# Kernel optimization log

Measured on AMD Instinct MI355X. Metric: run time of the kernel, lower is better.

The kernel has to match this reference:

```python
import jax, jax.numpy as jnp
import numpy as np

B, T, C = 2, 2048, 1024
H, D = 16, 64


def setup_inputs() -> dict:
    key = jax.random.key(0)
    ks = jax.random.split(key, 6)
    s = 0.02
    return {
        "x": jax.random.normal(ks[0], (B, T, C), dtype=jnp.float32),
        "W_qkv": jax.random.normal(ks[1], (3 * H * D, C), dtype=jnp.float32) * s,
        "b_qkv": jnp.zeros((3 * H * D,), dtype=jnp.float32),
        "W_proj": jax.random.normal(ks[2], (C, H * D), dtype=jnp.float32) * s,
        "b_proj": jnp.zeros((C,), dtype=jnp.float32),
        "sink_logit": jnp.zeros((H,), dtype=jnp.float32),
    }


def reference(x, W_qkv, b_qkv, W_proj, b_proj, sink_logit):
    Bx, Tx, Cx = x.shape
    qkv = x @ W_qkv.T + b_qkv  # (B,T,3*H*D)
    q, k, v = jnp.split(qkv, 3, axis=-1)
    # (B,T,H,D) -> (B,H,T,D)
    q = q.reshape(Bx, Tx, H, D).transpose(0, 2, 1, 3)
    k = k.reshape(Bx, Tx, H, D).transpose(0, 2, 1, 3)
    v = v.reshape(Bx, Tx, H, D).transpose(0, 2, 1, 3)
    scale = 1.0 / jnp.sqrt(jnp.asarray(D, dtype=x.dtype))
    scores = jnp.einsum("bhqd,bhkd->bhqk", q, k) * scale  # (B,H,T,T)
    neg_inf = jnp.finfo(x.dtype).min
    causal = jnp.tril(jnp.ones((Tx, Tx), dtype=bool))
    scores = jnp.where(causal[None, None], scores, neg_inf)
    # sink slot: k_sink = 0 so its logit is just the learnable sink bias
    sink = jnp.broadcast_to(sink_logit[None, :, None, None], (Bx, H, Tx, 1))
    logits = jnp.concatenate([sink.astype(scores.dtype), scores], axis=-1)  # (B,H,T,T+1)
    probs = jax.nn.softmax(logits, axis=-1)
    # v_sink is zero, so drop sink column in the value contraction
    out = jnp.einsum("bhqk,bhkd->bhqd", probs[..., 1:], v)
    y = out.transpose(0, 2, 1, 3).reshape(Bx, Tx, H * D)
    return y @ W_proj.T + b_proj
```

## Files before the change

### kernel.cpp

```cpp
#include <hip/hip_runtime.h>
#include <hip/hip_bf16.h>

#define Bb 2
#define Tt 2048
#define Cc 1024
#define Hh 16
#define Dd 64

typedef __bf16 bf8 __attribute__((ext_vector_type(8)));
typedef __bf16 bf4 __attribute__((ext_vector_type(4)));
typedef float f4 __attribute__((ext_vector_type(4)));

typedef __attribute__((address_space(3))) void lds_void;
typedef const __attribute__((address_space(1))) void g_void;

__device__ __forceinline__ void gload_lds16(const __bf16* g, __bf16* l) {
  __builtin_amdgcn_global_load_lds((g_void*)g, (lds_void*)l, 16, 0, 0);
}

__device__ __forceinline__ float ex2(float x) { return __builtin_amdgcn_exp2f(x); }

__global__ __launch_bounds__(256) void cvt3_kernel(
    const float* __restrict__ a, __bf16* __restrict__ oa, int na,
    const float* __restrict__ b, __bf16* __restrict__ ob, int nb,
    const float* __restrict__ c, __bf16* __restrict__ oc) {
  int gi = blockIdx.x * 256 + threadIdx.x;
  const int t0 = na >> 3, t1 = t0 + (nb >> 3);
  const float* src; __bf16* dst; int idx;
  if (gi < t0)      { src = a; dst = oa; idx = gi; }
  else if (gi < t1) { src = b; dst = ob; idx = gi - t0; }
  else              { src = c; dst = oc; idx = gi - t1; }
  const float* p = src + (size_t)idx * 8;
  float4 u = *(const float4*)p;
  float4 v = *(const float4*)(p + 4);
  bf8 r;
  r[0] = (__bf16)u.x; r[1] = (__bf16)u.y; r[2] = (__bf16)u.z; r[3] = (__bf16)u.w;
  r[4] = (__bf16)v.x; r[5] = (__bf16)v.y; r[6] = (__bf16)v.z; r[7] = (__bf16)v.w;
  *(bf8*)(dst + (size_t)idx * 8) = r;
}

__global__ __launch_bounds__(256) void gemm128_kernel(
    const __bf16* __restrict__ A, const __bf16* __restrict__ W,
    const float* __restrict__ bias, int K, int mode,
    __bf16* __restrict__ q_ws, __bf16* __restrict__ k_ws,
    __bf16* __restrict__ v_ws, float* __restrict__ out, int ldo)
{
  const int tid = threadIdx.x;
  const int lane = tid & 63, wave = tid >> 6;
  const int lr = lane & 15, lq = lane >> 4;
  const int m_blk = blockIdx.y * 128, n_blk = blockIdx.x * 128;
  const int wm = (wave & 1) * 64, wn = (wave >> 1) * 64;

  __shared__ __align__(16) __bf16 As[128 * 32];
  __shared__ __align__(16) __bf16 Bs[128 * 32];

  const int srow = tid >> 2, scol = (tid & 3) * 8;
  const __bf16* ag0 = A + (size_t)(m_blk + srow) * K + scol;
  const __bf16* ag1 = A + (size_t)(m_blk + 64 + srow) * K + scol;
  const __bf16* bg0 = W + (size_t)(n_blk + srow) * K + scol;
  const __bf16* bg1 = W + (size_t)(n_blk + 64 + srow) * K + scol;
  __bf16* al0 = As + tid * 8;
  __bf16* al1 = As + 2048 + tid * 8;
  __bf16* bl0 = Bs + tid * 8;
  __bf16* bl1 = Bs + 2048 + tid * 8;

  f4 acc[4][4] = {};
  for (int k0 = 0; k0 < K; k0 += 32) {
    gload_lds16(ag0 + k0, al0);
    gload_lds16(ag1 + k0, al1);
    gload_lds16(bg0 + k0, bl0);
    gload_lds16(bg1 + k0, bl1);
    __syncthreads();

    bf8 af[4], bfr[4];
    #pragma unroll
    for (int i = 0; i < 4; ++i)
      af[i] = *(const bf8*)&As[(wm + i * 16 + lr) * 32 + lq * 8];
    #pragma unroll
    for (int j = 0; j < 4; ++j)
      bfr[j] = *(const bf8*)&Bs[(wn + j * 16 + lr) * 32 + lq * 8];
    #pragma unroll
    for (int i = 0; i < 4; ++i)
      #pragma unroll
      for (int j = 0; j < 4; ++j)
        acc[i][j] = __builtin_amdgcn_mfma_f32_16x16x32_bf16(af[i], bfr[j], acc[i][j], 0, 0, 0);
    __syncthreads();
  }

  #pragma unroll
  for (int i = 0; i < 4; ++i) {
    #pragma unroll
    for (int j = 0; j < 4; ++j) {
      #pragma unroll
      for (int r = 0; r < 4; ++r) {
        int row = m_blk + wm + i * 16 + lq * 4 + r;
        int col = n_blk + wn + j * 16 + lr;
        float val = acc[i][j][r] + bias[col];
        if (mode == 0) {
          int which = col >> 10, rr = col & 1023;
          int h = rr >> 6, d = rr & 63;
          int b = row >> 11, t = row & 2047;
          if (which == 0) val *= 0.18033688011112042f;
          __bf16 bv = (__bf16)val;
          size_t bh = (size_t)b * Hh + h;
          if (which == 0)      q_ws[(bh * Tt + t) * Dd + d] = bv;
          else if (which == 1) k_ws[(bh * Tt + t) * Dd + d] = bv;
          else                 v_ws[(bh * Dd + d) * Tt + t] = bv;
        } else {
          out[(size_t)row * ldo + col] = val;
        }
      }
    }
  }
}

__global__ __launch_bounds__(256) void attn_kernel(
    const __bf16* __restrict__ q_ws, const __bf16* __restrict__ k_ws,
    const __bf16* __restrict__ v_ws, const float* __restrict__ sink,
    __bf16* __restrict__ y_ws)
{
  int bi = blockIdx.x;
  int qt, bhi;
  if (bi < 256) { qt = 15 - (bi >> 5); bhi = bi & 31; }
  else          { qt = (bi - 256) >> 5; bhi = (bi - 256) & 31; }
  const int h = bhi & (Hh - 1);
  const int b = bhi >> 4;
  const int tid = threadIdx.x;
  const int lane = tid & 63, wave = tid >> 6;
  const int lr = lane & 15, lq = lane >> 4;

  __shared__ __align__(16) __bf16 KsU[3][64 * 64];
  __shared__ __align__(16) __bf16 VtU[3][64 * 64];
  __shared__ __align__(16) __bf16 PsU[4][2 * 16 * 64];

  const __bf16* qp = q_ws + (size_t)bhi * Tt * Dd;
  const __bf16* kp = k_ws + (size_t)bhi * Tt * Dd;
  const __bf16* vp = v_ws + (size_t)bhi * Dd * Tt;

  const int qbase = qt * 128;
  const int qlo = qbase + wave * 32;

  bf8 qf[2][2];
  #pragma unroll
  for (int qs = 0; qs < 2; ++qs) {
    const __bf16* qrow = qp + (size_t)(qlo + qs * 16 + lr) * Dd;
    qf[qs][0] = *(const bf8*)(qrow + lq * 8);
    qf[qs][1] = *(const bf8*)(qrow + 32 + lq * 8);
  }

  float rs[2] = {0.f, 0.f};
  f4 o_acc[2][4] = {};

  const int srow_lo = wave * 8 + (lane >> 3);
  const int sslot = lane & 7;
  const int nkt = 2 * qt + 2;

  auto stage = [&](int kt2, int bsel) {
    const int kbase2 = kt2 * 64;
    #pragma unroll
    for (int ii = 0; ii < 2; ++ii) {
      const int r = ii * 32 + srow_lo;
      const int cc = sslot ^ (r & 7);
      gload_lds16(kp + (size_t)(kbase2 + r) * Dd + cc * 8,
                  &KsU[bsel][ii * 2048 + wave * 512 + lane * 8]);
      gload_lds16(vp + (size_t)r * Tt + kbase2 + cc * 8,
                  &VtU[bsel][ii * 2048 + wave * 512 + lane * 8]);
    }
  };

  auto computeS = [&](const __bf16* Kb, f4 (&sA)[4][2]) {
    #pragma unroll
    for (int nt = 0; nt < 4; ++nt) {
      const int krow = nt * 16 + lr;
      const int x7 = krow & 7;
      bf8 kb0 = *(const bf8*)&Kb[krow * 64 + ((lq ^ x7) * 8)];
      bf8 kb1 = *(const bf8*)&Kb[krow * 64 + (((4 + lq) ^ x7) * 8)];
      #pragma unroll
      for (int qs = 0; qs < 2; ++qs) {
        f4 c = {};
        c = __builtin_amdgcn_mfma_f32_16x16x32_bf16(kb0, qf[qs][0], c, 0, 0, 0);
        c = __builtin_amdgcn_mfma_f32_16x16x32_bf16(kb1, qf[qs][1], c, 0, 0, 0);
        sA[nt][qs] = c;
      }
    }
  };

  f4 s_cur[4][2], s_next[4][2];

  stage(0, 0);
  __syncthreads();
  stage(1, 1);
  computeS(KsU[0], s_cur);

  for (int kt = 0; kt < nkt; ++kt) {
    __syncthreads();
    if (kt + 2 < nkt) stage(kt + 2, (kt + 2) % 3);

    if (kt + 1 < nkt && (kt + 1) * 64 <= qlo + 31)
      computeS(KsU[(kt + 1) % 3], s_next);

    const int kbase = kt * 64;
    if (kbase <= qlo + 31) {
      __bf16* Pw = PsU[wave];
      const bool diag = (kbase + 63 > qlo);
      if (diag) {
        #pragma unroll
        for (int nt = 0; nt < 4; ++nt)
          #pragma unroll
          for (int qs = 0; qs < 2; ++qs) {
            const int qg = qlo + qs * 16 + lr;
            const int kg = kbase + nt * 16 + lq * 4;
            bf4 pb;
            #pragma unroll
            for (int r = 0; r < 4; ++r) {
              float sv = (kg + r > qg) ? -1e30f : s_cur[nt][qs][r];
              float p = ex2(sv);
              rs[qs] += p;
              pb[r] = (__bf16)p;
            }
            const int G = (nt * 2 + (lq >> 1)) ^ (lr & 7);
            *(bf4*)&Pw[(qs * 16 + lr) * 64 + G * 8 + (lq & 1) * 4] = pb;
          }
      } else {
        #pragma unroll
        for (int nt = 0; nt < 4; ++nt)
          #pragma unroll
          for (int qs = 0; qs < 2; ++qs) {
            bf4 pb;
            #pragma unroll
            for (int r = 0; r < 4; ++r) {
              float p = ex2(s_cur[nt][qs][r]);
              rs[qs] += p;
              pb[r] = (__bf16)p;
            }
            const int G = (nt * 2 + (lq >> 1)) ^ (lr & 7);
            *(bf4*)&Pw[(qs * 16 + lr) * 64 + G * 8 + (lq & 1) * 4] = pb;
          }
      }
      asm volatile("s_waitcnt lgkmcnt(0)" ::: "memory");

      const __bf16* Vb = VtU[kt % 3];
      #pragma unroll
      for (int ks = 0; ks < 2; ++ks) {
        const int pg = ((ks * 4 + lq) ^ (lr & 7)) * 8;
        bf8 pa0 = *(const bf8*)&Pw[lr * 64 + pg];
        bf8 pa1 = *(const bf8*)&Pw[(16 + lr) * 64 + pg];
        #pragma unroll
        for (int dt = 0; dt < 4; ++dt) {
          const int vrow = dt * 16 + lr;
          bf8 vb = *(const bf8*)&Vb[vrow * 64 + (((ks * 4 + lq) ^ (vrow & 7)) * 8)];
          o_acc[0][dt] = __builtin_amdgcn_mfma_f32_16x16x32_bf16(pa0, vb, o_acc[0][dt], 0, 0, 0);
          o_acc[1][dt] = __builtin_amdgcn_mfma_f32_16x16x32_bf16(pa1, vb, o_acc[1][dt], 0, 0, 0);
        }
      }
    }

    #pragma unroll
    for (int nt = 0; nt < 4; ++nt)
      #pragma unroll
      for (int qs = 0; qs < 2; ++qs)
        s_cur[nt][qs] = s_next[nt][qs];
  }

  #pragma unroll
  for (int qs = 0; qs < 2; ++qs) {
    rs[qs] += __shfl_xor(rs[qs], 16, 64);
    rs[qs] += __shfl_xor(rs[qs], 32, 64);
  }
  const float snk = ex2(sink[h] * 1.44269504f);
  float inv0 = 1.0f / (rs[0] + snk);
  float inv1 = 1.0f / (rs[1] + snk);
  float invr[2][4];
  #pragma unroll
  for (int r = 0; r < 4; ++r) {
    invr[0][r] = __shfl(inv0, lq * 4 + r, 64);
    invr[1][r] = __shfl(inv1, lq * 4 + r, 64);
  }

  #pragma unroll
  for (int qs = 0; qs < 2; ++qs)
    #pragma unroll
    for (int dt = 0; dt < 4; ++dt)
      #pragma unroll
      for (int r = 0; r < 4; ++r) {
        int qrow = qbase + wave * 32 + qs * 16 + lq * 4 + r;
        y_ws[((size_t)b * Tt + qrow) * Cc + h * Dd + dt * 16 + lr] =
            (__bf16)(o_acc[qs][dt][r] * invr[qs][r]);
      }
}

extern "C" void kernel_launch(void* const* d_in, const int* in_sizes, int n_in,
                              void* d_out, int out_size, void* d_ws, size_t ws_size,
                              hipStream_t stream) {
  const float* x      = (const float*)d_in[0];
  const float* W_qkv  = (const float*)d_in[1];
  const float* b_qkv  = (const float*)d_in[2];
  const float* W_proj = (const float*)d_in[3];
  const float* b_proj = (const float*)d_in[4];
  const float* sinkp  = (const float*)d_in[5];
  float* out = (float*)d_out;

  const size_t n_x    = (size_t)Bb * Tt * Cc;
  const size_t n_wqkv = (size_t)3 * Hh * Dd * Cc;
  const size_t n_wprj = (size_t)Cc * Hh * Dd;
  const size_t nqkv   = (size_t)Bb * Hh * Tt * Dd;

  __bf16* xb     = (__bf16*)d_ws;
  __bf16* wqkvb  = xb + n_x;
  __bf16* wprojb = wqkvb + n_wqkv;
  __bf16* q_ws   = wprojb + n_wprj;
  __bf16* k_ws   = q_ws + nqkv;
  __bf16* v_ws   = k_ws + nqkv;
  __bf16* y_ws   = xb;

  dim3 blk(256);
  const int cvt_blocks = (int)((n_x + n_wqkv + n_wprj) / 8 / 256);
  cvt3_kernel<<<cvt_blocks, blk, 0, stream>>>(x, xb, (int)n_x,
                                              W_qkv, wqkvb, (int)n_wqkv,
                                              W_proj, wprojb);

  gemm128_kernel<<<dim3(3 * Cc / 128, Bb * Tt / 128), blk, 0, stream>>>(
      xb, wqkvb, b_qkv, Cc, 0, q_ws, k_ws, v_ws, nullptr, 0);
  attn_kernel<<<dim3(512), blk, 0, stream>>>(q_ws, k_ws, v_ws, sinkp, y_ws);
  gemm128_kernel<<<dim3(Cc / 128, Bb * Tt / 128), blk, 0, stream>>>(
      y_ws, wprojb, b_proj, Hh * Dd, 1, nullptr, nullptr, nullptr, out, Cc);
}
```

Before: 203.7 us.

## Double-buffer GEMM LDS tiles, swizzle LDS layout, use 64-row tiles for projection

```diff
diff --git a/kernel.cpp b/kernel.cpp
--- a/kernel.cpp
+++ b/kernel.cpp
@@ -39,64 +39,87 @@
   *(bf8*)(dst + (size_t)idx * 8) = r;
 }
 
-__global__ __launch_bounds__(256) void gemm128_kernel(
+template<int BM, int BN, int MODE>
+__global__ __launch_bounds__(256) void gemm_kernel(
     const __bf16* __restrict__ A, const __bf16* __restrict__ W,
-    const float* __restrict__ bias, int K, int mode,
+    const float* __restrict__ bias, int K,
     __bf16* __restrict__ q_ws, __bf16* __restrict__ k_ws,
     __bf16* __restrict__ v_ws, float* __restrict__ out, int ldo)
 {
+  constexpr int WM = (BM == 128) ? 64 : 32;
+  constexpr int WN = 64;
+  constexpr int WAVES_M = BM / WM;
+  constexpr int MI = WM / 16, NI = WN / 16;
+  constexpr int NA = BM / 64, NB = BN / 64;
+
   const int tid = threadIdx.x;
   const int lane = tid & 63, wave = tid >> 6;
   const int lr = lane & 15, lq = lane >> 4;
-  const int m_blk = blockIdx.y * 128, n_blk = blockIdx.x * 128;
-  const int wm = (wave & 1) * 64, wn = (wave >> 1) * 64;
-
-  __shared__ __align__(16) __bf16 As[128 * 32];
-  __shared__ __align__(16) __bf16 Bs[128 * 32];
-
-  const int srow = tid >> 2, scol = (tid & 3) * 8;
-  const __bf16* ag0 = A + (size_t)(m_blk + srow) * K + scol;
-  const __bf16* ag1 = A + (size_t)(m_blk + 64 + srow) * K + scol;
-  const __bf16* bg0 = W + (size_t)(n_blk + srow) * K + scol;
-  const __bf16* bg1 = W + (size_t)(n_blk + 64 + srow) * K + scol;
-  __bf16* al0 = As + tid * 8;
-  __bf16* al1 = As + 2048 + tid * 8;
-  __bf16* bl0 = Bs + tid * 8;
-  __bf16* bl1 = Bs + 2048 + tid * 8;
-
-  f4 acc[4][4] = {};
-  for (int k0 = 0; k0 < K; k0 += 32) {
-    gload_lds16(ag0 + k0, al0);
-    gload_lds16(ag1 + k0, al1);
-    gload_lds16(bg0 + k0, bl0);
-    gload_lds16(bg1 + k0, bl1);
+  const int m_blk = blockIdx.y * BM, n_blk = blockIdx.x * BN;
+  const int wm = (wave % WAVES_M) * WM, wn = (wave / WAVES_M) * WN;
+
+  __shared__ __align__(16) __bf16 As[2][BM * 32];
+  __shared__ __align__(16) __bf16 Bs[2][BN * 32];
+
+  const int scol = ((tid & 3) ^ ((tid >> 3) & 3)) * 8;
+  const __bf16* agp[NA];
+  const __bf16* bgp[NB];
+  #pragma unroll
+  for (int i = 0; i < NA; ++i)
+    agp[i] = A + (size_t)(m_blk + i * 64 + (tid >> 2)) * K + scol;
+  #pragma unroll
+  for (int i = 0; i < NB; ++i)
+    bgp[i] = W + (size_t)(n_blk + i * 64 + (tid >> 2)) * K + scol;
+
+  const int nk = K >> 5;
+
+  auto stage = [&](int k, int bsel) {
+    #pragma unroll
+    for (int i = 0; i < NA; ++i)
+      gload_lds16(agp[i] + k * 32, &As[bsel][i * 2048 + tid * 8]);
+    #pragma unroll
+    for (int i = 0; i < NB; ++i)
+      gload_lds16(bgp[i] + k * 32, &Bs[bsel][i * 2048 + tid * 8]);
+  };
+
+  f4 acc[MI][NI] = {};
+  const int xsw = (lr >> 1) & 3;
+
+  auto compute = [&](const __bf16* Ab, const __bf16* Bw) {
+    bf8 af[MI], bfr[NI];
+    #pragma unroll
+    for (int i = 0; i < MI; ++i)
+      af[i] = *(const bf8*)&Ab[(wm + i * 16 + lr) * 32 + ((lq ^ xsw) * 8)];
+    #pragma unroll
+    for (int j = 0; j < NI; ++j)
+      bfr[j] = *(const bf8*)&Bw[(wn + j * 16 + lr) * 32 + ((lq ^ xsw) * 8)];
+    #pragma unroll
+    for (int i = 0; i < MI; ++i)
+      #pragma unroll
+      for (int j = 0; j < NI; ++j)
+        acc[i][j] = __builtin_amdgcn_mfma_f32_16x16x32_bf16(af[i], bfr[j], acc[i][j], 0, 0, 0);
+  };
+
+  stage(0, 0);
+  for (int k = 0; k + 2 <= nk; k += 2) {
     __syncthreads();
-
-    bf8 af[4], bfr[4];
-    #pragma unroll
-    for (int i = 0; i < 4; ++i)
-      af[i] = *(const bf8*)&As[(wm + i * 16 + lr) * 32 + lq * 8];
-    #pragma unroll
-    for (int j = 0; j < 4; ++j)
-      bfr[j] = *(const bf8*)&Bs[(wn + j * 16 + lr) * 32 + lq * 8];
-    #pragma unroll
-    for (int i = 0; i < 4; ++i)
-      #pragma unroll
-      for (int j = 0; j < 4; ++j)
-        acc[i][j] = __builtin_amdgcn_mfma_f32_16x16x32_bf16(af[i], bfr[j], acc[i][j], 0, 0, 0);
+    if (k + 1 < nk) stage(k + 1, 1);
+    compute(As[0], Bs[0]);
     __syncthreads();
-  }
-
-  #pragma unroll
-  for (int i = 0; i < 4; ++i) {
-    #pragma unroll
-    for (int j = 0; j < 4; ++j) {
+    if (k + 2 < nk) stage(k + 2, 0);
+    compute(As[1], Bs[1]);
+  }
+
+  #pragma unroll
+  for (int i = 0; i < MI; ++i) {
+    #pragma unroll
+    for (int j = 0; j < NI; ++j) {
       #pragma unroll
       for (int r = 0; r < 4; ++r) {
         int row = m_blk + wm + i * 16 + lq * 4 + r;
         int col = n_blk + wn + j * 16 + lr;
         float val = acc[i][j][r] + bias[col];
-        if (mode == 0) {
+        if constexpr (MODE == 0) {
           int which = col >> 10, rr = col & 1023;
           int h = rr >> 6, d = rr & 63;
           int b = row >> 11, t = row & 2047;
@@ -319,9 +342,9 @@
                                               W_qkv, wqkvb, (int)n_wqkv,
                                               W_proj, wprojb);
 
-  gemm128_kernel<<<dim3(3 * Cc / 128, Bb * Tt / 128), blk, 0, stream>>>(
-      xb, wqkvb, b_qkv, Cc, 0, q_ws, k_ws, v_ws, nullptr, 0);
+  gemm_kernel<128, 128, 0><<<dim3(3 * Cc / 128, Bb * Tt / 128), blk, 0, stream>>>(
+      xb, wqkvb, b_qkv, Cc, q_ws, k_ws, v_ws, nullptr, 0);
   attn_kernel<<<dim3(512), blk, 0, stream>>>(q_ws, k_ws, v_ws, sinkp, y_ws);
-  gemm128_kernel<<<dim3(Cc / 128, Bb * Tt / 128), blk, 0, stream>>>(
-      y_ws, wprojb, b_proj, Hh * Dd, 1, nullptr, nullptr, nullptr, out, Cc);
-}
+  gemm_kernel<64, 128, 1><<<dim3(Cc / 128, Bb * Tt / 64), blk, 0, stream>>>(
+      y_ws, wprojb, b_proj, Hh * Dd, nullptr, nullptr, nullptr, out, Cc);
+}
```

After: 209.7 us. 1.03x slower.

## Double-buffer GEMM LDS tiles and switch to 32x32x16 MFMA

Applied to the files above, without the earlier changes.

```diff
diff --git a/kernel.cpp b/kernel.cpp
--- a/kernel.cpp
+++ b/kernel.cpp
@@ -10,6 +10,7 @@
 typedef __bf16 bf8 __attribute__((ext_vector_type(8)));
 typedef __bf16 bf4 __attribute__((ext_vector_type(4)));
 typedef float f4 __attribute__((ext_vector_type(4)));
+typedef float f16v __attribute__((ext_vector_type(16)));
 
 typedef __attribute__((address_space(3))) void lds_void;
 typedef const __attribute__((address_space(1))) void g_void;
@@ -47,55 +48,67 @@
 {
   const int tid = threadIdx.x;
   const int lane = tid & 63, wave = tid >> 6;
-  const int lr = lane & 15, lq = lane >> 4;
+  const int l32 = lane & 31, lh = lane >> 5;
   const int m_blk = blockIdx.y * 128, n_blk = blockIdx.x * 128;
   const int wm = (wave & 1) * 64, wn = (wave >> 1) * 64;
 
-  __shared__ __align__(16) __bf16 As[128 * 32];
-  __shared__ __align__(16) __bf16 Bs[128 * 32];
+  __shared__ __align__(16) __bf16 As[2][128 * 32];
+  __shared__ __align__(16) __bf16 Bs[2][128 * 32];
 
   const int srow = tid >> 2, scol = (tid & 3) * 8;
   const __bf16* ag0 = A + (size_t)(m_blk + srow) * K + scol;
-  const __bf16* ag1 = A + (size_t)(m_blk + 64 + srow) * K + scol;
+  const __bf16* ag1 = ag0 + (size_t)64 * K;
   const __bf16* bg0 = W + (size_t)(n_blk + srow) * K + scol;
-  const __bf16* bg1 = W + (size_t)(n_blk + 64 + srow) * K + scol;
-  __bf16* al0 = As + tid * 8;
-  __bf16* al1 = As + 2048 + tid * 8;
-  __bf16* bl0 = Bs + tid * 8;
-  __bf16* bl1 = Bs + 2048 + tid * 8;
-
-  f4 acc[4][4] = {};
-  for (int k0 = 0; k0 < K; k0 += 32) {
-    gload_lds16(ag0 + k0, al0);
-    gload_lds16(ag1 + k0, al1);
-    gload_lds16(bg0 + k0, bl0);
-    gload_lds16(bg1 + k0, bl1);
+  const __bf16* bg1 = bg0 + (size_t)64 * K;
+
+  auto stage = [&](int k0, int bsel) {
+    gload_lds16(ag0 + k0, &As[bsel][tid * 8]);
+    gload_lds16(ag1 + k0, &As[bsel][2048 + tid * 8]);
+    gload_lds16(bg0 + k0, &Bs[bsel][tid * 8]);
+    gload_lds16(bg1 + k0, &Bs[bsel][2048 + tid * 8]);
+  };
+
+  f16v acc[2][2] = {};
+
+  auto compute = [&](const __bf16* Ab, const __bf16* Bw) {
+    #pragma unroll
+    for (int ks = 0; ks < 2; ++ks) {
+      bf8 af[2], bfr[2];
+      #pragma unroll
+      for (int mt = 0; mt < 2; ++mt)
+        af[mt] = *(const bf8*)&Ab[(wm + mt * 32 + l32) * 32 + ks * 16 + lh * 8];
+      #pragma unroll
+      for (int nt = 0; nt < 2; ++nt)
+        bfr[nt] = *(const bf8*)&Bw[(wn + nt * 32 + l32) * 32 + ks * 16 + lh * 8];
+      #pragma unroll
+      for (int mt = 0; mt < 2; ++mt)
+        #pragma unroll
+        for (int nt = 0; nt < 2; ++nt)
+          acc[mt][nt] = __builtin_amdgcn_mfma_f32_32x32x16_bf16(
+              af[mt], bfr[nt], acc[mt][nt], 0, 0, 0);
+    }
+  };
+
+  const int nk = K >> 5;
+  stage(0, 0);
+  for (int k = 0; k + 2 <= nk; k += 2) {
     __syncthreads();
-
-    bf8 af[4], bfr[4];
-    #pragma unroll
-    for (int i = 0; i < 4; ++i)
-      af[i] = *(const bf8*)&As[(wm + i * 16 + lr) * 32 + lq * 8];
-    #pragma unroll
-    for (int j = 0; j < 4; ++j)
-      bfr[j] = *(const bf8*)&Bs[(wn + j * 16 + lr) * 32 + lq * 8];
-    #pragma unroll
-    for (int i = 0; i < 4; ++i)
-      #pragma unroll
-      for (int j = 0; j < 4; ++j)
-        acc[i][j] = __builtin_amdgcn_mfma_f32_16x16x32_bf16(af[i], bfr[j], acc[i][j], 0, 0, 0);
+    if (k + 1 < nk) stage((k + 1) * 32, 1);
+    compute(As[0], Bs[0]);
     __syncthreads();
-  }
-
-  #pragma unroll
-  for (int i = 0; i < 4; ++i) {
-    #pragma unroll
-    for (int j = 0; j < 4; ++j) {
-      #pragma unroll
-      for (int r = 0; r < 4; ++r) {
-        int row = m_blk + wm + i * 16 + lq * 4 + r;
-        int col = n_blk + wn + j * 16 + lr;
-        float val = acc[i][j][r] + bias[col];
+    if (k + 2 < nk) stage((k + 2) * 32, 0);
+    compute(As[1], Bs[1]);
+  }
+
+  #pragma unroll
+  for (int mt = 0; mt < 2; ++mt) {
+    #pragma unroll
+    for (int nt = 0; nt < 2; ++nt) {
+      #pragma unroll
+      for (int reg = 0; reg < 16; ++reg) {
+        int row = m_blk + wm + mt * 32 + 4 * lh + (reg & 3) + 8 * (reg >> 2);
+        int col = n_blk + wn + nt * 32 + l32;
+        float val = acc[mt][nt][reg] + bias[col];
         if (mode == 0) {
           int which = col >> 10, rr = col & 1023;
           int h = rr >> 6, d = rr & 63;
```

Result: no change. 202.6 us (-0.5%).

## Transpose V through LDS in QKV epilogue; use 64x64 tiles for output projection

Applied to the files above, without the earlier changes.

```diff
diff --git a/kernel.cpp b/kernel.cpp
--- a/kernel.cpp
+++ b/kernel.cpp
@@ -41,9 +41,9 @@
 
 __global__ __launch_bounds__(256) void gemm128_kernel(
     const __bf16* __restrict__ A, const __bf16* __restrict__ W,
-    const float* __restrict__ bias, int K, int mode,
+    const float* __restrict__ bias, int K,
     __bf16* __restrict__ q_ws, __bf16* __restrict__ k_ws,
-    __bf16* __restrict__ v_ws, float* __restrict__ out, int ldo)
+    __bf16* __restrict__ v_ws)
 {
   const int tid = threadIdx.x;
   const int lane = tid & 63, wave = tid >> 6;
@@ -53,6 +53,7 @@
 
   __shared__ __align__(16) __bf16 As[128 * 32];
   __shared__ __align__(16) __bf16 Bs[128 * 32];
+  __shared__ __align__(16) __bf16 Epi[4][64 * 72];
 
   const int srow = tid >> 2, scol = (tid & 3) * 8;
   const __bf16* ag0 = A + (size_t)(m_blk + srow) * K + scol;
@@ -87,31 +88,102 @@
     __syncthreads();
   }
 
-  #pragma unroll
-  for (int i = 0; i < 4; ++i) {
+  const int col0 = n_blk + wn;
+  const int which = col0 >> 10;
+  const int b = m_blk >> 11;
+  const int h = (col0 & 1023) >> 6;
+  const size_t bh = (size_t)b * Hh + h;
+
+  if (which == 2) {
+    __bf16* E = Epi[wave];
     #pragma unroll
     for (int j = 0; j < 4; ++j) {
+      float bv = bias[col0 + j * 16 + lr];
+      #pragma unroll
+      for (int i = 0; i < 4; ++i)
+        #pragma unroll
+        for (int r = 0; r < 4; ++r)
+          E[(j * 16 + lr) * 72 + i * 16 + lq * 4 + r] = (__bf16)(acc[i][j][r] + bv);
+    }
+    asm volatile("s_waitcnt lgkmcnt(0)" ::: "memory");
+    const int t0 = (m_blk + wm) & 2047;
+    const int dd = lane >> 3, tl = (lane & 7) * 8;
+    #pragma unroll
+    for (int di = 0; di < 8; ++di) {
+      int d = di * 8 + dd;
+      bf8 vv = *(const bf8*)&E[d * 72 + tl];
+      *(bf8*)&v_ws[(bh * Dd + d) * Tt + t0 + tl] = vv;
+    }
+  } else {
+    __bf16* dst = (which == 0) ? q_ws : k_ws;
+    const float scl = (which == 0) ? 0.18033688011112042f : 1.0f;
+    #pragma unroll
+    for (int i = 0; i < 4; ++i) {
+      #pragma unroll
+      for (int j = 0; j < 4; ++j) {
+        #pragma unroll
+        for (int r = 0; r < 4; ++r) {
+          int row = m_blk + wm + i * 16 + lq * 4 + r;
+          int col = col0 + j * 16 + lr;
+          float val = (acc[i][j][r] + bias[col]) * scl;
+          int d = col & 63, t = row & 2047;
+          dst[(bh * Tt + t) * Dd + d] = (__bf16)val;
+        }
+      }
+    }
+  }
+}
+
+__global__ __launch_bounds__(256) void gemm64_kernel(
+    const __bf16* __restrict__ A, const __bf16* __restrict__ W,
+    const float* __restrict__ bias, int K, float* __restrict__ out, int ldo)
+{
+  const int tid = threadIdx.x;
+  const int lane = tid & 63, wave = tid >> 6;
+  const int lr = lane & 15, lq = lane >> 4;
+  const int m_blk = blockIdx.y * 64, n_blk = blockIdx.x * 64;
+  const int wm = (wave & 1) * 32, wn = (wave >> 1) * 32;
+
+  __shared__ __align__(16) __bf16 As[64 * 32];
+  __shared__ __align__(16) __bf16 Bs[64 * 32];
+
+  const int srow = tid >> 2, scol = (tid & 3) * 8;
+  const __bf16* ag = A + (size_t)(m_blk + srow) * K + scol;
+  const __bf16* bg = W + (size_t)(n_blk + srow) * K + scol;
+  __bf16* al = As + tid * 8;
+  __bf16* bl = Bs + tid * 8;
+
+  f4 acc[2][2] = {};
+  for (int k0 = 0; k0 < K; k0 += 32) {
+    gload_lds16(ag + k0, al);
+    gload_lds16(bg + k0, bl);
+    __syncthreads();
+
+    bf8 af[2], bfr[2];
+    #pragma unroll
+    for (int i = 0; i < 2; ++i)
+      af[i] = *(const bf8*)&As[(wm + i * 16 + lr) * 32 + lq * 8];
+    #pragma unroll
+    for (int j = 0; j < 2; ++j)
+      bfr[j] = *(const bf8*)&Bs[(wn + j * 16 + lr) * 32 + lq * 8];
+    #pragma unroll
+    for (int i = 0; i < 2; ++i)
+      #pragma unroll
+      for (int j = 0; j < 2; ++j)
+        acc[i][j] = __builtin_amdgcn_mfma_f32_16x16x32_bf16(af[i], bfr[j], acc[i][j], 0, 0, 0);
+    __syncthreads();
+  }
+
+  #pragma unroll
+  for (int i = 0; i < 2; ++i)
+    #pragma unroll
+    for (int j = 0; j < 2; ++j)
       #pragma unroll
       for (int r = 0; r < 4; ++r) {
         int row = m_blk + wm + i * 16 + lq * 4 + r;
         int col = n_blk + wn + j * 16 + lr;
-        float val = acc[i][j][r] + bias[col];
-        if (mode == 0) {
-          int which = col >> 10, rr = col & 1023;
-          int h = rr >> 6, d = rr & 63;
-          int b = row >> 11, t = row & 2047;
-          if (which == 0) val *= 0.18033688011112042f;
-          __bf16 bv = (__bf16)val;
-          size_t bh = (size_t)b * Hh + h;
-          if (which == 0)      q_ws[(bh * Tt + t) * Dd + d] = bv;
-          else if (which == 1) k_ws[(bh * Tt + t) * Dd + d] = bv;
-          else                 v_ws[(bh * Dd + d) * Tt + t] = bv;
-        } else {
-          out[(size_t)row * ldo + col] = val;
-        }
-      }
-    }
-  }
+        out[(size_t)row * ldo + col] = acc[i][j][r] + bias[col];
+      }
 }
 
 __global__ __launch_bounds__(256) void attn_kernel(
@@ -320,8 +392,8 @@
                                               W_proj, wprojb);
 
   gemm128_kernel<<<dim3(3 * Cc / 128, Bb * Tt / 128), blk, 0, stream>>>(
-      xb, wqkvb, b_qkv, Cc, 0, q_ws, k_ws, v_ws, nullptr, 0);
+      xb, wqkvb, b_qkv, Cc, q_ws, k_ws, v_ws);
   attn_kernel<<<dim3(512), blk, 0, stream>>>(q_ws, k_ws, v_ws, sinkp, y_ws);
-  gemm128_kernel<<<dim3(Cc / 128, Bb * Tt / 128), blk, 0, stream>>>(
-      y_ws, wprojb, b_proj, Hh * Dd, 1, nullptr, nullptr, nullptr, out, Cc);
-}
+  gemm64_kernel<<<dim3(Cc / 64, Bb * Tt / 64), blk, 0, stream>>>(
+      y_ws, wprojb, b_proj, Hh * Dd, out, Cc);
+}
```

Result: faster. 186.0 us (-8.7%).
